# Kernel tuning notes

Hardware: AMD Instinct MI355X
Metric: run time of the kernel (lower is better)

The kernel has to match this reference:

```python
import jax, jax.numpy as jnp
import numpy as np

B = 524288   # batch rows
K = 8        # number of BooleanClassifiers
I = 64       # n_inputs
H = 32       # n_hidden
SCALE = 1.0  # LinearNetwork.scale (default [1.0])


def setup_inputs() -> dict:
    key = jax.random.key(0)
    k_x, k_w1, k_b1, k_w2, k_b2 = jax.random.split(key, 5)
    return {
        "x": jax.random.normal(k_x, (B, I), dtype=jnp.float32),
        "W1": jax.random.normal(k_w1, (K, H, I), dtype=jnp.float32) * 0.1,
        "b1": jax.random.normal(k_b1, (K, H), dtype=jnp.float32) * 0.1,
        "W2": jax.random.normal(k_w2, (K, H), dtype=jnp.float32) * 0.1,
        "b2": jax.random.normal(k_b2, (K,), dtype=jnp.float32) * 0.1,
        "bias": jnp.zeros((K,), dtype=jnp.float32),  # unused in training-mode forward
    }


def reference(x, W1, b1, W2, b2, bias):
    # Loop of K tiny Linear-Tanh-Linear-Tanh classifiers, fused as batched GEMMs.
    # h: [B, K, H]
    h = jnp.tanh(jnp.einsum("bi,khi->bkh", x, W1) + b1)
    # per-classifier scalar output, concatenated along dim=1 -> [B, K]
    out = jnp.tanh(jnp.einsum("bkh,kh->bk", h, W2) + b2)
    out = out * SCALE                   # LinearNetwork scale
    out = (out + 1.0) * 0.5 * SCALE     # LinearWithTanh training branch
    return out
```

## Files before the change

### kernel.cpp

```cpp
#include <hip/hip_runtime.h>
#include <hip/hip_bf16.h>

typedef __attribute__((ext_vector_type(8))) short short8;
typedef __attribute__((ext_vector_type(4))) float f32x4;

constexpr int B_ROWS   = 524288;
constexpr int ROWTILES = B_ROWS / 64;
constexpr int GRID     = 2048;
constexpr float L2E2   = 2.8853900817779268f;

__device__ __forceinline__ short bf16_rne(float f) {
  union { float f; unsigned u; } v; v.f = f;
  unsigned u = v.u + 0x7FFFu + ((v.u >> 16) & 1u);
  return (short)(u >> 16);
}

__device__ __forceinline__ short8 pack8(f32x4 a, f32x4 b) {
  short8 f;
  f[0] = bf16_rne(a[0]); f[1] = bf16_rne(a[1]);
  f[2] = bf16_rne(a[2]); f[3] = bf16_rne(a[3]);
  f[4] = bf16_rne(b[0]); f[5] = bf16_rne(b[1]);
  f[6] = bf16_rne(b[2]); f[7] = bf16_rne(b[3]);
  return f;
}

__global__ __launch_bounds__(256, 4) void fused_mlp8(
    const float* __restrict__ x, const float* __restrict__ W1,
    const float* __restrict__ b1, const float* __restrict__ W2,
    const float* __restrict__ b2, float* __restrict__ out) {

  const int tid  = threadIdx.x;
  const int wave = tid >> 6;
  const int lane = tid & 63;
  const int m16  = lane & 15;
  const int q    = lane >> 4;

  short8 w1f[4][2];
#pragma unroll
  for (int mt = 0; mt < 4; ++mt) {
    const int n = (wave * 4 + mt) * 16 + m16;
#pragma unroll
    for (int ks = 0; ks < 2; ++ks) {
      const float* p = W1 + n * 64 + ks * 32 + q * 8;
      w1f[mt][ks] = pack8(*(const f32x4*)p, *(const f32x4*)(p + 4));
    }
  }

  f32x4 kb1[4], w2m[4];
  float sw2[2] = {0.f, 0.f};
#pragma unroll
  for (int mt = 0; mt < 4; ++mt) {
    const int n0 = (wave * 4 + mt) * 16 + q * 4;
    const f32x4 b1x = *(const f32x4*)(b1 + n0);
    const f32x4 w2x = *(const f32x4*)(W2 + n0);
#pragma unroll
    for (int r = 0; r < 4; ++r) {
      kb1[mt][r] = L2E2 * b1x[r];
      w2m[mt][r] = -2.0f * w2x[r];
      sw2[mt >> 1] += w2x[r];
    }
  }
  float KSb[2];
#pragma unroll
  for (int j = 0; j < 2; ++j) {
    float s = sw2[j];
    s += __shfl_xor(s, 16);
    s += __shfl_xor(s, 32);
    KSb[j] = L2E2 * (s + b2[wave * 2 + j]);
  }

  for (int it = blockIdx.x; it < ROWTILES; it += GRID) {
    const long base = (long)it * 64;

#pragma unroll
    for (int tt = 0; tt < 4; ++tt) {
      const float* rp = x + (base + tt * 16 + m16) * 64 + q * 8;
      const f32x4 a0 = *(const f32x4*)(rp);
      const f32x4 a1 = *(const f32x4*)(rp + 4);
      const f32x4 c0 = *(const f32x4*)(rp + 32);
      const f32x4 c1 = *(const f32x4*)(rp + 36);
      const short8 xf0 = pack8(a0, a1);
      const short8 xf1 = pack8(c0, c1);

      f32x4 acc[4];
#pragma unroll
      for (int mt = 0; mt < 4; ++mt) {
        f32x4 z = { 0.f, 0.f, 0.f, 0.f };
        z = __builtin_amdgcn_mfma_f32_16x16x32_bf16(w1f[mt][0], xf0, z, 0, 0, 0);
        z = __builtin_amdgcn_mfma_f32_16x16x32_bf16(w1f[mt][1], xf1, z, 0, 0, 0);
        acc[mt] = z;
      }

      float o0 = 0.f, o1 = 0.f;
#pragma unroll
      for (int j = 0; j < 2; ++j) {
        float P = 0.f;
#pragma unroll
        for (int t = 0; t < 2; ++t) {
          const int mt = j * 2 + t;
#pragma unroll
          for (int r = 0; r < 4; ++r) {
            const float e = __builtin_amdgcn_exp2f(
                __builtin_fmaf(acc[mt][r], L2E2, kb1[mt][r]));
            P = __builtin_fmaf(w2m[mt][r], __builtin_amdgcn_rcpf(e + 1.0f), P);
          }
        }
        P += __shfl_xor(P, 16);
        P += __shfl_xor(P, 32);
        const float arg = __builtin_fmaf(P, L2E2, KSb[j]);
        const float o = 1.0f - __builtin_amdgcn_rcpf(
            __builtin_amdgcn_exp2f(arg) + 1.0f);
        if (j == 0) o0 = o; else o1 = o;
      }

      if (q == 0) {
        float2 st; st.x = o0; st.y = o1;
        *(float2*)(out + (base + tt * 16 + m16) * 8 + wave * 2) = st;
      }
    }
  }
}

extern "C" void kernel_launch(void* const* d_in, const int* in_sizes, int n_in,
                              void* d_out, int out_size, void* d_ws, size_t ws_size,
                              hipStream_t stream) {
  const float* x  = (const float*)d_in[0];
  const float* W1 = (const float*)d_in[1];
  const float* b1 = (const float*)d_in[2];
  const float* W2 = (const float*)d_in[3];
  const float* b2 = (const float*)d_in[4];
  float* out = (float*)d_out;
  fused_mlp8<<<GRID, 256, 0, stream>>>(x, W1, b1, W2, b2, out);
}
```

Measured before the change: 235.4 us.

## Stage x tile through LDS with register prefetch and coalesced output stores

Each block now loads its 64-row x tile once, cooperatively and coalesced, converts it to bf16 and stores it into a swizzled shared buffer that all four waves read. Before, every wave reloaded and reconverted the whole tile. The next tile is prefetched into registers while the current one is computed. Outputs go through a shared staging buffer so global writes are contiguous. The change also folds the log2e scale into W1, uses a cheaper perm-based bf16 pack that rounds half-up instead of to nearest even, and adds two barriers per tile.

```diff
diff --git a/kernel.cpp b/kernel.cpp
--- a/kernel.cpp
+++ b/kernel.cpp
@@ -1,5 +1,4 @@
 #include <hip/hip_runtime.h>
-#include <hip/hip_bf16.h>
 
 typedef __attribute__((ext_vector_type(8))) short short8;
 typedef __attribute__((ext_vector_type(4))) float f32x4;
@@ -9,25 +8,28 @@
 constexpr int GRID     = 2048;
 constexpr float L2E2   = 2.8853900817779268f;
 
-__device__ __forceinline__ short bf16_rne(float f) {
-  union { float f; unsigned u; } v; v.f = f;
-  unsigned u = v.u + 0x7FFFu + ((v.u >> 16) & 1u);
-  return (short)(u >> 16);
+union V16 { uint4 u; short8 s; };
+
+__device__ __forceinline__ unsigned pk(float lo, float hi) {
+  const unsigned a = __float_as_uint(lo) + 0x8000u;
+  const unsigned b = __float_as_uint(hi) + 0x8000u;
+  return __builtin_amdgcn_perm(b, a, 0x07060302u);
 }
 
-__device__ __forceinline__ short8 pack8(f32x4 a, f32x4 b) {
-  short8 f;
-  f[0] = bf16_rne(a[0]); f[1] = bf16_rne(a[1]);
-  f[2] = bf16_rne(a[2]); f[3] = bf16_rne(a[3]);
-  f[4] = bf16_rne(b[0]); f[5] = bf16_rne(b[1]);
-  f[6] = bf16_rne(b[2]); f[7] = bf16_rne(b[3]);
-  return f;
+__device__ __forceinline__ V16 pk8(f32x4 a, f32x4 b) {
+  V16 v;
+  v.u.x = pk(a[0], a[1]); v.u.y = pk(a[2], a[3]);
+  v.u.z = pk(b[0], b[1]); v.u.w = pk(b[2], b[3]);
+  return v;
 }
 
 __global__ __launch_bounds__(256, 4) void fused_mlp8(
     const float* __restrict__ x, const float* __restrict__ W1,
     const float* __restrict__ b1, const float* __restrict__ W2,
     const float* __restrict__ b2, float* __restrict__ out) {
+
+  __shared__ V16 xbuf[512];
+  __shared__ float obuf[64 * 10];
 
   const int tid  = threadIdx.x;
   const int wave = tid >> 6;
@@ -42,7 +44,11 @@
 #pragma unroll
     for (int ks = 0; ks < 2; ++ks) {
       const float* p = W1 + n * 64 + ks * 32 + q * 8;
-      w1f[mt][ks] = pack8(*(const f32x4*)p, *(const f32x4*)(p + 4));
+      const f32x4 u0 = *(const f32x4*)p, u1 = *(const f32x4*)(p + 4);
+      f32x4 s0, s1;
+#pragma unroll
+      for (int r = 0; r < 4; ++r) { s0[r] = L2E2 * u0[r]; s1[r] = L2E2 * u1[r]; }
+      w1f[mt][ks] = pk8(s0, s1).s;
     }
   }
 
@@ -69,18 +75,34 @@
     KSb[j] = L2E2 * (s + b2[wave * 2 + j]);
   }
 
+  const int srow = tid >> 2;
+  const int seg  = tid & 3;
+  const int sw   = srow & 7;
+
+  f32x4 pf[4];
+  {
+    const float* gp = x + ((long)blockIdx.x * 64 + srow) * 64 + seg * 16;
+#pragma unroll
+    for (int c = 0; c < 4; ++c) pf[c] = *(const f32x4*)(gp + c * 4);
+  }
+
   for (int it = blockIdx.x; it < ROWTILES; it += GRID) {
-    const long base = (long)it * 64;
+    xbuf[srow * 8 + ((seg * 2)     ^ sw)] = pk8(pf[0], pf[1]);
+    xbuf[srow * 8 + ((seg * 2 + 1) ^ sw)] = pk8(pf[2], pf[3]);
+    __syncthreads();
+
+    if (it + GRID < ROWTILES) {
+      const float* gp = x + ((long)(it + GRID) * 64 + srow) * 64 + seg * 16;
+#pragma unroll
+      for (int c = 0; c < 4; ++c) pf[c] = *(const f32x4*)(gp + c * 4);
+    }
 
 #pragma unroll
     for (int tt = 0; tt < 4; ++tt) {
-      const float* rp = x + (base + tt * 16 + m16) * 64 + q * 8;
-      const f32x4 a0 = *(const f32x4*)(rp);
-      const f32x4 a1 = *(const f32x4*)(rp + 4);
-      const f32x4 c0 = *(const f32x4*)(rp + 32);
-      const f32x4 c1 = *(const f32x4*)(rp + 36);
-      const short8 xf0 = pack8(a0, a1);
-      const short8 xf1 = pack8(c0, c1);
+      const int r   = tt * 16 + m16;
+      const int rsw = r & 7;
+      const short8 xf0 = xbuf[r * 8 + (q       ^ rsw)].s;
+      const short8 xf1 = xbuf[r * 8 + ((q + 4) ^ rsw)].s;
 
       f32x4 acc[4];
 #pragma unroll
@@ -99,10 +121,9 @@
         for (int t = 0; t < 2; ++t) {
           const int mt = j * 2 + t;
 #pragma unroll
-          for (int r = 0; r < 4; ++r) {
-            const float e = __builtin_amdgcn_exp2f(
-                __builtin_fmaf(acc[mt][r], L2E2, kb1[mt][r]));
-            P = __builtin_fmaf(w2m[mt][r], __builtin_amdgcn_rcpf(e + 1.0f), P);
+          for (int rr = 0; rr < 4; ++rr) {
+            const float e = __builtin_amdgcn_exp2f(acc[mt][rr] + kb1[mt][rr]);
+            P = __builtin_fmaf(w2m[mt][rr], __builtin_amdgcn_rcpf(e + 1.0f), P);
           }
         }
         P += __shfl_xor(P, 16);
@@ -115,8 +136,15 @@
 
       if (q == 0) {
         float2 st; st.x = o0; st.y = o1;
-        *(float2*)(out + (base + tt * 16 + m16) * 8 + wave * 2) = st;
+        *(float2*)&obuf[r * 10 + wave * 2] = st;
       }
+    }
+    __syncthreads();
+
+    {
+      const int orow = tid >> 2, oc = (tid & 3) * 2;
+      const float2 v = *(const float2*)&obuf[orow * 10 + oc];
+      *(float2*)(out + ((long)it * 64 + orow) * 8 + oc) = v;
     }
   }
 }
```

New measurement: 208.9 us. 1.13x faster.
